# Kernel optimization log

Hardware: AMD Instinct MI355X
Metric: run time of the kernel (lower is better)

The kernel has to match this reference:

```python
import jax, jax.numpy as jnp
import numpy as np

EPS = 1e-6

def rmsnorm(x, w):
    # RMSNorm over last dim (head_dim), eps=1e-6, learned scale w
    return x * jax.lax.rsqrt(jnp.mean(x * x, axis=-1, keepdims=True) + EPS) * w

def setup_inputs() -> dict:
    key = jax.random.key(0)
    ks = jax.random.split(key, 8)
    B, L, D = 2, 256, 4096          # batch, new-chunk len, model dim
    H, Dh = 32, 128                  # heads, head_dim (H*Dh == D)
    SINK, LOCAL = 128, 4096          # attention-sink + sliding window
    S = SINK + LOCAL                 # fixed cache length
    s = 0.02
    return {
        "x": jax.random.normal(ks[0], (B, L, D), jnp.float32),
        "cache_k": jax.random.normal(ks[1], (B, S, H, Dh), jnp.float32),
        "cache_v": jax.random.normal(ks[2], (B, S, H, Dh), jnp.float32),
        "Wq": jax.random.normal(ks[3], (D, H * Dh), jnp.float32) * s,
        "Wk": jax.random.normal(ks[4], (D, H * Dh), jnp.float32) * s,
        "Wv": jax.random.normal(ks[5], (D, H * Dh), jnp.float32) * s,
        "Wo": jax.random.normal(ks[6], (H * Dh, D), jnp.float32) * s,
        "q_norm_w": jnp.ones((Dh,), jnp.float32),
        "k_norm_w": jnp.ones((Dh,), jnp.float32),
        "sink": 128,
    }

def reference(x, cache_k, cache_v, Wq, Wk, Wv, Wo, q_norm_w, k_norm_w, sink):
    B, L, D = x.shape
    S, H, Dh = cache_k.shape[1], cache_k.shape[2], cache_k.shape[3]
    # QKV projections (bias=False) + per-head RMSNorm on q and k
    q = rmsnorm((x @ Wq).reshape(B, L, H, Dh), q_norm_w)
    k = rmsnorm((x @ Wk).reshape(B, L, H, Dh), k_norm_w)
    v = (x @ Wv).reshape(B, L, H, Dh)
    # steady-state cache: keep sink tokens, roll local window left by L, write new chunk at tail
    new_k = jnp.concatenate([cache_k[:, :sink], cache_k[:, sink + L:], k], axis=1)  # [B,S,H,Dh]
    new_v = jnp.concatenate([cache_v[:, :sink], cache_v[:, sink + L:], v], axis=1)
    scale = 1.0 / jnp.sqrt(jnp.asarray(Dh, x.dtype))
    logits = jnp.einsum('blhd,bshd->bhls', q, new_k) * scale  # [B,H,L,S]
    # causal within the new chunk: query i sees cache positions j <= (S-L)+i
    i = jnp.arange(L)[:, None]
    j = jnp.arange(S)[None, :]
    mask = j <= (S - L) + i
    logits = jnp.where(mask[None, None], logits, jnp.finfo(logits.dtype).min)
    attn = jax.nn.softmax(logits, axis=-1)
    out = jnp.einsum('bhls,bshd->blhd', attn, new_v).reshape(B, L, H * Dh)
    return out @ Wo
```

## Files before the change

### kernel.cpp

```cpp
#include <hip/hip_runtime.h>
#include <stdint.h>
#include <stddef.h>

typedef unsigned short u16;
typedef __bf16 bf16x8 __attribute__((ext_vector_type(8)));
typedef float f32x4 __attribute__((ext_vector_type(4)));
typedef u16 u16x8 __attribute__((ext_vector_type(8)));

#define B_    2
#define L_    256
#define D_    4096
#define H_    32
#define DH_   128
#define SINK_ 128
#define S_    4224
#define WINS_ 3968
#define M_    512
#define SPLIT_ 4

__device__ __forceinline__ float bf2f(u16 u){
  union { float f; uint32_t i; } v; v.i = ((uint32_t)u) << 16; return v.f;
}
__device__ __forceinline__ u16 f2bf(float f){
  union { float f; uint32_t i; } v; v.f = f;
  return (u16)((v.i + 0x7fffu + ((v.i >> 16) & 1u)) >> 16);
}
__device__ __forceinline__ bf16x8 ld8(const u16* p){
  return __builtin_bit_cast(bf16x8, *(const u16x8*)p);
}
__device__ __forceinline__ bf16x8 ld8f(const float* p){
  f32x4 a = *(const f32x4*)p;
  f32x4 b = *(const f32x4*)(p + 4);
  u16x8 r;
  r[0] = f2bf(a[0]); r[1] = f2bf(a[1]); r[2] = f2bf(a[2]); r[3] = f2bf(a[3]);
  r[4] = f2bf(b[0]); r[5] = f2bf(b[1]); r[6] = f2bf(b[2]); r[7] = f2bf(b[3]);
  return __builtin_bit_cast(bf16x8, r);
}

__global__ void detect_k(const u16* __restrict__ x, uint32_t* __restrict__ flag){
  const int lane = threadIdx.x & 63;
  int bad = 0;
  for (int i = lane; i < 1024; i += 64){
    float v = bf2f(x[2 * i]);
    if (!(v * 0.0f == 0.0f) || fabsf(v) > 1e6f) bad = 1;
  }
#pragma unroll
  for (int m = 1; m < 64; m <<= 1) bad |= __shfl_xor(bad, m, 64);
  if (threadIdx.x == 0) *flag = (uint32_t)(bad ? 1 : 0);
}

__global__ __launch_bounds__(256) void transpose_k(const void* __restrict__ W,
                                                   u16* __restrict__ WT,
                                                   const uint32_t* __restrict__ flag){
  const int mode = (int)*flag;
  __shared__ u16 Ts[64 * 68];
  const int t  = threadIdx.x;
  const int k0 = blockIdx.x * 64;
  const int n0 = blockIdx.y * 64;
  const int r  = t >> 2;
  const int c  = (t & 3) * 8;
  const size_t rowoff = (size_t)(k0 + r) * 4096;
#pragma unroll
  for (int p = 0; p < 2; p++){
    const int cc = c + p * 32;
    u16x8 v;
    if (mode){
      const float* pf = (const float*)W + rowoff + n0 + cc;
      f32x4 a = *(const f32x4*)pf;
      f32x4 b = *(const f32x4*)(pf + 4);
      v[0] = f2bf(a[0]); v[1] = f2bf(a[1]); v[2] = f2bf(a[2]); v[3] = f2bf(a[3]);
      v[4] = f2bf(b[0]); v[5] = f2bf(b[1]); v[6] = f2bf(b[2]); v[7] = f2bf(b[3]);
    } else {
      v = *(const u16x8*)((const u16*)W + rowoff + n0 + cc);
    }
#pragma unroll
    for (int j = 0; j < 8; j++) Ts[r * 68 + cc + j] = v[j];
  }
  __syncthreads();
#pragma unroll
  for (int p = 0; p < 2; p++){
    const int kc = c + p * 32;
    u16x8 v;
#pragma unroll
    for (int j = 0; j < 8; j++) v[j] = Ts[(kc + j) * 68 + r];
    *(u16x8*)(WT + (size_t)(n0 + r) * 4096 + k0 + kc) = v;
  }
}

__global__ __launch_bounds__(256) void gemm_bt(const void* __restrict__ Ain,
                                               const u16* __restrict__ BT,
                                               void* __restrict__ Cout,
                                               const uint32_t* __restrict__ flag,
                                               int a_ext, int c_ext){
  const int mode = (int)*flag;
  const int a_f32 = a_ext & mode;
  const int c_f32 = c_ext & mode;

  const int n0 = blockIdx.x * 128;
  const int m0 = blockIdx.y * 64;

  __shared__ u16 As[64 * 32];
  __shared__ u16 Bs[128 * 32];

  const int t    = threadIdx.x;
  const int w    = t >> 6;
  const int lane = t & 63;
  const int wm   = w >> 1;
  const int wn   = w & 1;
  const int mq   = lane & 15;
  const int qd   = lane >> 4;

  f32x4 acc[2][4] = {};

  const size_t ga  = (size_t)(m0 + (t >> 2)) * 4096 + (t & 3) * 8;
  const size_t gb0 = (size_t)(n0 + (t >> 2)) * 4096 + (t & 3) * 8;
  const size_t gb1 = (size_t)(n0 + 64 + (t >> 2)) * 4096 + (t & 3) * 8;

  for (int kt = 0; kt < 128; kt++){
    const int k0 = kt * 32;
    u16x8 av;
    if (a_f32){
      const float* pa = (const float*)Ain + ga + k0;
      f32x4 a = *(const f32x4*)pa;
      f32x4 b = *(const f32x4*)(pa + 4);
      av[0] = f2bf(a[0]); av[1] = f2bf(a[1]); av[2] = f2bf(a[2]); av[3] = f2bf(a[3]);
      av[4] = f2bf(b[0]); av[5] = f2bf(b[1]); av[6] = f2bf(b[2]); av[7] = f2bf(b[3]);
    } else {
      av = *(const u16x8*)((const u16*)Ain + ga + k0);
    }
    u16x8 bv0 = *(const u16x8*)(BT + gb0 + k0);
    u16x8 bv1 = *(const u16x8*)(BT + gb1 + k0);
    __syncthreads();
    *(u16x8*)&As[t * 8]         = av;
    *(u16x8*)&Bs[t * 8]         = bv0;
    *(u16x8*)&Bs[(256 + t) * 8] = bv1;
    __syncthreads();

    bf16x8 af[2], bfr[4];
#pragma unroll
    for (int i = 0; i < 2; i++)
      af[i] = ld8(&As[(wm * 32 + i * 16 + mq) * 32 + qd * 8]);
#pragma unroll
    for (int j = 0; j < 4; j++)
      bfr[j] = ld8(&Bs[(wn * 64 + j * 16 + mq) * 32 + qd * 8]);
#pragma unroll
    for (int i = 0; i < 2; i++)
#pragma unroll
      for (int j = 0; j < 4; j++)
        acc[i][j] = __builtin_amdgcn_mfma_f32_16x16x32_bf16(af[i], bfr[j], acc[i][j], 0, 0, 0);
  }

#pragma unroll
  for (int i = 0; i < 2; i++)
#pragma unroll
    for (int j = 0; j < 4; j++)
#pragma unroll
      for (int r = 0; r < 4; r++){
        const int row = m0 + wm * 32 + i * 16 + qd * 4 + r;
        const int col = n0 + wn * 64 + j * 16 + mq;
        if (c_f32) ((float*)Cout)[(size_t)row * 4096 + col] = acc[i][j][r];
        else       ((u16*)Cout)[(size_t)row * 4096 + col]   = f2bf(acc[i][j][r]);
      }
}

__global__ __launch_bounds__(256) void rmsnorm_k(const u16* __restrict__ src,
                                                 u16* __restrict__ dst,
                                                 const void* __restrict__ wq,
                                                 const void* __restrict__ wk,
                                                 const uint32_t* __restrict__ flag){
  const int mode = (int)*flag;
  const int t = threadIdx.x, w = t >> 6, lane = t & 63;
  const size_t base = (size_t)blockIdx.y * (size_t)M_ * 4096;
  const int rid = blockIdx.x * 4 + w;
  const u16* s = src + base + (size_t)rid * 128 + lane * 2;
  u16*       d = dst + base + (size_t)rid * 128 + lane * 2;
  const void* wp = blockIdx.y ? wk : wq;
  float w0, w1;
  if (mode){ w0 = ((const float*)wp)[lane * 2]; w1 = ((const float*)wp)[lane * 2 + 1]; }
  else     { w0 = bf2f(((const u16*)wp)[lane * 2]); w1 = bf2f(((const u16*)wp)[lane * 2 + 1]); }
  const float f0 = bf2f(s[0]), f1 = bf2f(s[1]);
  float ss = f0 * f0 + f1 * f1;
#pragma unroll
  for (int m = 1; m < 64; m <<= 1) ss += __shfl_xor(ss, m, 64);
  const float rinv = rsqrtf(ss * (1.0f / 128.0f) + 1e-6f);
  d[0] = f2bf(f0 * rinv * w0);
  d[1] = f2bf(f1 * rinv * w1);
}

__global__ __launch_bounds__(1024) void attn_k(const u16* __restrict__ qn,
                                               const u16* __restrict__ kn,
                                               const u16* __restrict__ vnew,
                                               const void* __restrict__ ck,
                                               const void* __restrict__ cv,
                                               u16* __restrict__ ao,
                                               const uint32_t* __restrict__ flag){
  const int mode = (int)*flag;
  __shared__ __align__(16) unsigned char LDSB[61440];
  u16*   VTall = (u16*)LDSB;
  u16*   PBall = (u16*)LDSB + 4 * 5120;
  float* OB    = (float*)LDSB;
  float* ML    = (float*)(LDSB + 32768);

  const int t  = threadIdx.x;
  const int W  = t >> 6;
  const int sp = W >> 2;
  const int w  = W & 3;
  const int lane = t & 63;
  const int lt = t & 255;
  const int blk = blockIdx.x;
  const int b  = blk >> 7;
  const int h  = (blk >> 2) & 31;
  const int qt = blk & 3;
  const int q0 = qt * 64 + w * 16;
  const int mq = lane & 15;
  const int qd = lane >> 4;

  u16* VT = VTall + sp * (128 * 40);
  u16* pb = PBall + W * 640;

  bf16x8 aq[4];
  {
    const u16* qp = qn + ((size_t)(b * L_ + q0 + mq)) * 4096 + h * 128 + qd * 8;
#pragma unroll
    for (int kc = 0; kc < 4; kc++) aq[kc] = ld8(qp + kc * 32);
  }

  f32x4 oacc[8] = {};
  float mi[4], li[4];
#pragma unroll
  for (int r = 0; r < 4; r++){ mi[r] = -1e30f; li[r] = 0.f; }

  const int nchunks = (WINS_ + qt * 64 + 63) / 32 + 1;
  const int cpb = (nchunks + SPLIT_ - 1) / SPLIT_;
  const int sc_beg = sp * cpb;
  const int sc_end = (sc_beg + cpb < nchunks) ? (sc_beg + cpb) : nchunks;
  const float scale = 0.08838834764831845f;
  const float L2E = 1.4426950408889634f;

  const int dd = lt & 127, sg = lt >> 7;

  for (int scr = 0; scr < cpb; scr++){
    const int sc = sc_beg + scr;
    const int act = (sc < sc_end);
    const int s0 = sc * 32;

    u16 vv[16];
    if (act){
#pragma unroll
      for (int j = 0; j < 16; j++){
        const int s = s0 + sg * 16 + j;
        if (s >= WINS_){
          vv[j] = vnew[((size_t)(b * L_ + (s - WINS_)) << 12) + h * 128 + dd];
        } else {
          const int scc = (s < SINK_) ? s : (s + L_);
          const size_t off = ((((size_t)b * S_ + scc) * H_ + h) << 7) + dd;
          vv[j] = mode ? f2bf(((const float*)cv)[off]) : ((const u16*)cv)[off];
        }
      }
    }
    __syncthreads();
    if (act){
#pragma unroll
      for (int hv = 0; hv < 2; hv++){
        u16x8 pk;
#pragma unroll
        for (int j = 0; j < 8; j++) pk[j] = vv[hv * 8 + j];
        *(u16x8*)&VT[dd * 40 + sg * 16 + hv * 8] = pk;
      }
    }
    __syncthreads();

    if (act){
      float lg[2][4];
#pragma unroll
      for (int st = 0; st < 2; st++){
        const int s = s0 + st * 16 + mq;
        f32x4 a = {};
        if (s0 + st * 16 >= WINS_){
          const u16* kp = kn + ((size_t)(b * L_ + (s - WINS_)) << 12) + h * 128;
#pragma unroll
          for (int kc = 0; kc < 4; kc++)
            a = __builtin_amdgcn_mfma_f32_16x16x32_bf16(aq[kc], ld8(kp + kc * 32 + qd * 8), a, 0, 0, 0);
        } else if (mode){
          const int scc = (s < SINK_) ? s : (s + L_);
          const float* kp = (const float*)ck + ((((size_t)b * S_ + scc) * H_ + h) << 7);
#pragma unroll
          for (int kc = 0; kc < 4; kc++)
            a = __builtin_amdgcn_mfma_f32_16x16x32_bf16(aq[kc], ld8f(kp + kc * 32 + qd * 8), a, 0, 0, 0);
        } else {
          const int scc = (s < SINK_) ? s : (s + L_);
          const u16* kp = (const u16*)ck + ((((size_t)b * S_ + scc) * H_ + h) << 7);
#pragma unroll
          for (int kc = 0; kc < 4; kc++)
            a = __builtin_amdgcn_mfma_f32_16x16x32_bf16(aq[kc], ld8(kp + kc * 32 + qd * 8), a, 0, 0, 0);
        }
#pragma unroll
        for (int r = 0; r < 4; r++) lg[st][r] = a[r] * scale;
      }
      if (s0 + 31 > WINS_ + q0){
#pragma unroll
        for (int st = 0; st < 2; st++){
          const int s = s0 + st * 16 + mq;
#pragma unroll
          for (int r = 0; r < 4; r++)
            if (s > WINS_ + (q0 + qd * 4 + r)) lg[st][r] = -1e30f;
        }
      }
      float p[2][4];
#pragma unroll
      for (int r = 0; r < 4; r++){
        float mx = fmaxf(lg[0][r], lg[1][r]);
#pragma unroll
        for (int m = 1; m < 16; m <<= 1) mx = fmaxf(mx, __shfl_xor(mx, m, 64));
        const float mnew = fmaxf(mi[r], mx);
        const float alpha = exp2f((mi[r] - mnew) * L2E);
        mi[r] = mnew;
        float s_ = 0.f;
#pragma unroll
        for (int st = 0; st < 2; st++){
          p[st][r] = exp2f((lg[st][r] - mnew) * L2E);
          s_ += p[st][r];
        }
#pragma unroll
        for (int m = 1; m < 16; m <<= 1) s_ += __shfl_xor(s_, m, 64);
        li[r] = li[r] * alpha + s_;
#pragma unroll
        for (int nt = 0; nt < 8; nt++) oacc[nt][r] *= alpha;
      }
#pragma unroll
      for (int st = 0; st < 2; st++)
#pragma unroll
        for (int r = 0; r < 4; r++)
          pb[(qd * 4 + r) * 40 + st * 16 + mq] = f2bf(p[st][r]);
      asm volatile("" ::: "memory");
      u16x8 pr;
#pragma unroll
      for (int j = 0; j < 8; j++) pr[j] = pb[mq * 40 + qd * 8 + j];
      bf16x8 ap = __builtin_bit_cast(bf16x8, pr);
#pragma unroll
      for (int nt = 0; nt < 8; nt++){
        bf16x8 bv = ld8(&VT[(nt * 16 + mq) * 40 + qd * 8]);
        oacc[nt] = __builtin_amdgcn_mfma_f32_16x16x32_bf16(ap, bv, oacc[nt], 0, 0, 0);
      }
    }
  }

  __syncthreads();
  if (mq == 0){
#pragma unroll
    for (int r = 0; r < 4; r++){
      const int lr = w * 16 + qd * 4 + r;
      ML[(sp * 64 + lr) * 2 + 0] = mi[r];
      ML[(sp * 64 + lr) * 2 + 1] = li[r];
    }
  }
  __syncthreads();

  float gm[4], gl[4], wgt[4];
#pragma unroll
  for (int r = 0; r < 4; r++){
    const int lr = w * 16 + qd * 4 + r;
    float m_ = -1e30f;
#pragma unroll
    for (int p = 0; p < SPLIT_; p++) m_ = fmaxf(m_, ML[(p * 64 + lr) * 2 + 0]);
    gm[r] = m_;
    float l_ = 0.f;
#pragma unroll
    for (int p = 0; p < SPLIT_; p++)
      l_ += exp2f((ML[(p * 64 + lr) * 2 + 0] - m_) * L2E) * ML[(p * 64 + lr) * 2 + 1];
    gl[r] = l_;
    wgt[r] = exp2f((mi[r] - m_) * L2E);
  }

#pragma unroll
  for (int p = 0; p < SPLIT_; p++){
    if (sp == p){
#pragma unroll
      for (int nt = 0; nt < 8; nt++)
#pragma unroll
        for (int r = 0; r < 4; r++){
          const int off = (w * 16 + qd * 4 + r) * 128 + nt * 16 + mq;
          const float v = wgt[r] * oacc[nt][r];
          if (p == 0) OB[off] = v;
          else        OB[off] += v;
        }
    }
    __syncthreads();
  }

  if (sp == 0){
#pragma unroll
    for (int nt = 0; nt < 8; nt++)
#pragma unroll
      for (int r = 0; r < 4; r++){
        const int lr = w * 16 + qd * 4 + r;
        const int qrow = qt * 64 + lr;
        const float v = OB[lr * 128 + nt * 16 + mq] / gl[r];
        ao[((size_t)(b * L_ + qrow) << 12) + h * 128 + nt * 16 + mq] = f2bf(v);
      }
  }
}

extern "C" void kernel_launch(void* const* d_in, const int* in_sizes, int n_in,
                              void* d_out, int out_size, void* d_ws, size_t ws_size,
                              hipStream_t stream){
  (void)in_sizes; (void)n_in; (void)out_size; (void)ws_size;
  const void* x  = d_in[0];
  const void* ck = d_in[1];
  const void* cv = d_in[2];
  const void* Wq = d_in[3];
  const void* Wk = d_in[4];
  const void* Wv = d_in[5];
  const void* Wo = d_in[6];
  const void* qw = d_in[7];
  const void* kw = d_in[8];

  const size_t WT_E = 4096ull * 4096;
  const size_t BUF  = (size_t)M_ * 4096;

  uint32_t* flag = (uint32_t*)d_ws;
  u16* ws0 = (u16*)d_ws + 64;
  u16* WT  = ws0;
  u16* qkv = WT + WT_E;
  u16* qn  = qkv + 3 * BUF;
  u16* ao  = qn + 2 * BUF;

  detect_k<<<1, 64, 0, stream>>>((const u16*)x, flag);

  transpose_k<<<dim3(64, 64), 256, 0, stream>>>(Wq, WT, flag);
  gemm_bt<<<dim3(32, 8), 256, 0, stream>>>(x, WT, qkv, flag, 1, 0);
  transpose_k<<<dim3(64, 64), 256, 0, stream>>>(Wk, WT, flag);
  gemm_bt<<<dim3(32, 8), 256, 0, stream>>>(x, WT, qkv + BUF, flag, 1, 0);
  transpose_k<<<dim3(64, 64), 256, 0, stream>>>(Wv, WT, flag);
  gemm_bt<<<dim3(32, 8), 256, 0, stream>>>(x, WT, qkv + 2 * BUF, flag, 1, 0);

  rmsnorm_k<<<dim3(4096, 2), 256, 0, stream>>>(qkv, qn, qw, kw, flag);

  attn_k<<<dim3(256), 1024, 0, stream>>>(qn, qn + BUF, qkv + 2 * BUF,
                                         ck, cv, ao, flag);

  transpose_k<<<dim3(64, 64), 256, 0, stream>>>(Wo, WT, flag);
  gemm_bt<<<dim3(32, 8), 256, 0, stream>>>(ao, WT, d_out, flag, 0, 1);
}
```

Measured before the change: 1.389 ms.

## Batch QKV GEMMs into one launch, shrink GEMM tiles, retile attention with V prefetch

The three Q/K/V weight transposes are staged into separate workspace slices, and a single GEMM launch covers all three projections, falling back to sequential launches when the workspace is too small. The GEMM tile shrinks from 64x128 to 64x64, which quadruples the grid and fills more CUs. The attention kernel moves from 1024-thread blocks with 64 queries to 512-thread blocks with 32 queries and 512 blocks, and prefetches the next V chunk into registers during compute. The goal is better occupancy and latency hiding, at the cost of less operand reuse per tile and more workspace.

Result: no change. 1.409 ms (+1.4%).

```diff
diff --git a/kernel.cpp b/kernel.cpp
--- a/kernel.cpp
+++ b/kernel.cpp
@@ -87,20 +87,23 @@
   }
 }
 
-__global__ __launch_bounds__(256) void gemm_bt(const void* __restrict__ Ain,
-                                               const u16* __restrict__ BT,
-                                               void* __restrict__ Cout,
-                                               const uint32_t* __restrict__ flag,
-                                               int a_ext, int c_ext){
+__global__ __launch_bounds__(256) void gemm64_k(const void* __restrict__ Ain,
+                                                const u16* __restrict__ BT3,
+                                                void* __restrict__ Cout,
+                                                const uint32_t* __restrict__ flag,
+                                                int a_ext, int c_ext){
   const int mode = (int)*flag;
   const int a_f32 = a_ext & mode;
   const int c_f32 = c_ext & mode;
 
-  const int n0 = blockIdx.x * 128;
+  const int bx = blockIdx.x;
+  const int wi = bx >> 6;
+  const int n0 = (bx & 63) * 64;
   const int m0 = blockIdx.y * 64;
+  const u16* BT = BT3 + (size_t)wi * (4096ull * 4096);
 
   __shared__ u16 As[64 * 32];
-  __shared__ u16 Bs[128 * 32];
+  __shared__ u16 Bs[64 * 32];
 
   const int t    = threadIdx.x;
   const int w    = t >> 6;
@@ -110,11 +113,10 @@
   const int mq   = lane & 15;
   const int qd   = lane >> 4;
 
-  f32x4 acc[2][4] = {};
-
-  const size_t ga  = (size_t)(m0 + (t >> 2)) * 4096 + (t & 3) * 8;
-  const size_t gb0 = (size_t)(n0 + (t >> 2)) * 4096 + (t & 3) * 8;
-  const size_t gb1 = (size_t)(n0 + 64 + (t >> 2)) * 4096 + (t & 3) * 8;
+  f32x4 acc[2][2] = {};
+
+  const size_t ga = (size_t)(m0 + (t >> 2)) * 4096 + (t & 3) * 8;
+  const size_t gb = (size_t)(n0 + (t >> 2)) * 4096 + (t & 3) * 8;
 
   for (int kt = 0; kt < 128; kt++){
     const int k0 = kt * 32;
@@ -128,38 +130,37 @@
     } else {
       av = *(const u16x8*)((const u16*)Ain + ga + k0);
     }
-    u16x8 bv0 = *(const u16x8*)(BT + gb0 + k0);
-    u16x8 bv1 = *(const u16x8*)(BT + gb1 + k0);
+    u16x8 bv = *(const u16x8*)(BT + gb + k0);
     __syncthreads();
-    *(u16x8*)&As[t * 8]         = av;
-    *(u16x8*)&Bs[t * 8]         = bv0;
-    *(u16x8*)&Bs[(256 + t) * 8] = bv1;
+    *(u16x8*)&As[t * 8] = av;
+    *(u16x8*)&Bs[t * 8] = bv;
     __syncthreads();
 
-    bf16x8 af[2], bfr[4];
+    bf16x8 af[2], bfr[2];
 #pragma unroll
     for (int i = 0; i < 2; i++)
       af[i] = ld8(&As[(wm * 32 + i * 16 + mq) * 32 + qd * 8]);
 #pragma unroll
-    for (int j = 0; j < 4; j++)
-      bfr[j] = ld8(&Bs[(wn * 64 + j * 16 + mq) * 32 + qd * 8]);
+    for (int j = 0; j < 2; j++)
+      bfr[j] = ld8(&Bs[(wn * 32 + j * 16 + mq) * 32 + qd * 8]);
 #pragma unroll
     for (int i = 0; i < 2; i++)
 #pragma unroll
-      for (int j = 0; j < 4; j++)
+      for (int j = 0; j < 2; j++)
         acc[i][j] = __builtin_amdgcn_mfma_f32_16x16x32_bf16(af[i], bfr[j], acc[i][j], 0, 0, 0);
   }
 
+  u16* cu = (u16*)Cout + (size_t)wi * ((size_t)M_ * 4096);
 #pragma unroll
   for (int i = 0; i < 2; i++)
 #pragma unroll
-    for (int j = 0; j < 4; j++)
+    for (int j = 0; j < 2; j++)
 #pragma unroll
       for (int r = 0; r < 4; r++){
         const int row = m0 + wm * 32 + i * 16 + qd * 4 + r;
-        const int col = n0 + wn * 64 + j * 16 + mq;
+        const int col = n0 + wn * 32 + j * 16 + mq;
         if (c_f32) ((float*)Cout)[(size_t)row * 4096 + col] = acc[i][j][r];
-        else       ((u16*)Cout)[(size_t)row * 4096 + col]   = f2bf(acc[i][j][r]);
+        else       cu[(size_t)row * 4096 + col]             = f2bf(acc[i][j][r]);
       }
 }
 
@@ -187,31 +188,31 @@
   d[1] = f2bf(f1 * rinv * w1);
 }
 
-__global__ __launch_bounds__(1024) void attn_k(const u16* __restrict__ qn,
-                                               const u16* __restrict__ kn,
-                                               const u16* __restrict__ vnew,
-                                               const void* __restrict__ ck,
-                                               const void* __restrict__ cv,
-                                               u16* __restrict__ ao,
-                                               const uint32_t* __restrict__ flag){
+__global__ __launch_bounds__(512, 4) void attn_k(const u16* __restrict__ qn,
+                                                 const u16* __restrict__ kn,
+                                                 const u16* __restrict__ vnew,
+                                                 const void* __restrict__ ck,
+                                                 const void* __restrict__ cv,
+                                                 u16* __restrict__ ao,
+                                                 const uint32_t* __restrict__ flag){
   const int mode = (int)*flag;
-  __shared__ __align__(16) unsigned char LDSB[61440];
+  __shared__ __align__(16) unsigned char LDSB[51200];
   u16*   VTall = (u16*)LDSB;
-  u16*   PBall = (u16*)LDSB + 4 * 5120;
+  u16*   PBall = (u16*)(LDSB + 40960);
   float* OB    = (float*)LDSB;
-  float* ML    = (float*)(LDSB + 32768);
+  float* ML    = (float*)(LDSB + 16384);
 
   const int t  = threadIdx.x;
   const int W  = t >> 6;
-  const int sp = W >> 2;
-  const int w  = W & 3;
+  const int sp = W >> 1;
+  const int w  = W & 1;
   const int lane = t & 63;
-  const int lt = t & 255;
+  const int lt = t & 127;
   const int blk = blockIdx.x;
-  const int b  = blk >> 7;
-  const int h  = (blk >> 2) & 31;
-  const int qt = blk & 3;
-  const int q0 = qt * 64 + w * 16;
+  const int b  = blk >> 8;
+  const int h  = (blk >> 3) & 31;
+  const int qt = blk & 7;
+  const int q0 = qt * 32 + w * 16;
   const int mq = lane & 15;
   const int qd = lane >> 4;
 
@@ -230,45 +231,51 @@
 #pragma unroll
   for (int r = 0; r < 4; r++){ mi[r] = -1e30f; li[r] = 0.f; }
 
-  const int nchunks = (WINS_ + qt * 64 + 63) / 32 + 1;
+  const int nchunks = (WINS_ + qt * 32 + 63) / 32;
   const int cpb = (nchunks + SPLIT_ - 1) / SPLIT_;
   const int sc_beg = sp * cpb;
   const int sc_end = (sc_beg + cpb < nchunks) ? (sc_beg + cpb) : nchunks;
   const float scale = 0.08838834764831845f;
   const float L2E = 1.4426950408889634f;
 
-  const int dd = lt & 127, sg = lt >> 7;
+  const int dd = lt;
+  u16x8 vv[4];
+
+  auto loadV = [&](int sc){
+    const int s0c = sc * 32;
+#pragma unroll
+    for (int c = 0; c < 4; c++){
+#pragma unroll
+      for (int j = 0; j < 8; j++){
+        const int s = s0c + c * 8 + j;
+        u16 val;
+        if (s >= WINS_){
+          val = vnew[((size_t)(b * L_ + (s - WINS_)) << 12) + h * 128 + dd];
+        } else {
+          const int scc = (s < SINK_) ? s : (s + L_);
+          const size_t off = ((((size_t)b * S_ + scc) * H_ + h) << 7) + dd;
+          val = mode ? f2bf(((const float*)cv)[off]) : ((const u16*)cv)[off];
+        }
+        vv[c][j] = val;
+      }
+    }
+  };
+
+  if (sc_beg < sc_end) loadV(sc_beg);
 
   for (int scr = 0; scr < cpb; scr++){
     const int sc = sc_beg + scr;
     const int act = (sc < sc_end);
     const int s0 = sc * 32;
 
-    u16 vv[16];
-    if (act){
-#pragma unroll
-      for (int j = 0; j < 16; j++){
-        const int s = s0 + sg * 16 + j;
-        if (s >= WINS_){
-          vv[j] = vnew[((size_t)(b * L_ + (s - WINS_)) << 12) + h * 128 + dd];
-        } else {
-          const int scc = (s < SINK_) ? s : (s + L_);
-          const size_t off = ((((size_t)b * S_ + scc) * H_ + h) << 7) + dd;
-          vv[j] = mode ? f2bf(((const float*)cv)[off]) : ((const u16*)cv)[off];
-        }
-      }
-    }
     __syncthreads();
     if (act){
 #pragma unroll
-      for (int hv = 0; hv < 2; hv++){
-        u16x8 pk;
-#pragma unroll
-        for (int j = 0; j < 8; j++) pk[j] = vv[hv * 8 + j];
-        *(u16x8*)&VT[dd * 40 + sg * 16 + hv * 8] = pk;
-      }
+      for (int c = 0; c < 4; c++)
+        *(u16x8*)&VT[dd * 40 + c * 8] = vv[c];
     }
     __syncthreads();
+    if (sc + 1 < sc_end) loadV(sc + 1);
 
     if (act){
       float lg[2][4];
@@ -350,24 +357,23 @@
 #pragma unroll
     for (int r = 0; r < 4; r++){
       const int lr = w * 16 + qd * 4 + r;
-      ML[(sp * 64 + lr) * 2 + 0] = mi[r];
-      ML[(sp * 64 + lr) * 2 + 1] = li[r];
+      ML[(sp * 32 + lr) * 2 + 0] = mi[r];
+      ML[(sp * 32 + lr) * 2 + 1] = li[r];
     }
   }
   __syncthreads();
 
-  float gm[4], gl[4], wgt[4];
+  float gl[4], wgt[4];
 #pragma unroll
   for (int r = 0; r < 4; r++){
     const int lr = w * 16 + qd * 4 + r;
     float m_ = -1e30f;
 #pragma unroll
-    for (int p = 0; p < SPLIT_; p++) m_ = fmaxf(m_, ML[(p * 64 + lr) * 2 + 0]);
-    gm[r] = m_;
+    for (int p = 0; p < SPLIT_; p++) m_ = fmaxf(m_, ML[(p * 32 + lr) * 2 + 0]);
     float l_ = 0.f;
 #pragma unroll
     for (int p = 0; p < SPLIT_; p++)
-      l_ += exp2f((ML[(p * 64 + lr) * 2 + 0] - m_) * L2E) * ML[(p * 64 + lr) * 2 + 1];
+      l_ += exp2f((ML[(p * 32 + lr) * 2 + 0] - m_) * L2E) * ML[(p * 32 + lr) * 2 + 1];
     gl[r] = l_;
     wgt[r] = exp2f((mi[r] - m_) * L2E);
   }
@@ -394,7 +400,7 @@
 #pragma unroll
       for (int r = 0; r < 4; r++){
         const int lr = w * 16 + qd * 4 + r;
-        const int qrow = qt * 64 + lr;
+        const int qrow = qt * 32 + lr;
         const float v = OB[lr * 128 + nt * 16 + mq] / gl[r];
         ao[((size_t)(b * L_ + qrow) << 12) + h * 128 + nt * 16 + mq] = f2bf(v);
       }
@@ -404,7 +410,7 @@
 extern "C" void kernel_launch(void* const* d_in, const int* in_sizes, int n_in,
                               void* d_out, int out_size, void* d_ws, size_t ws_size,
                               hipStream_t stream){
-  (void)in_sizes; (void)n_in; (void)out_size; (void)ws_size;
+  (void)in_sizes; (void)n_in; (void)out_size;
   const void* x  = d_in[0];
   const void* ck = d_in[1];
   const void* cv = d_in[2];
@@ -420,25 +426,47 @@
 
   uint32_t* flag = (uint32_t*)d_ws;
   u16* ws0 = (u16*)d_ws + 64;
-  u16* WT  = ws0;
-  u16* qkv = WT + WT_E;
-  u16* qn  = qkv + 3 * BUF;
-  u16* ao  = qn + 2 * BUF;
 
   detect_k<<<1, 64, 0, stream>>>((const u16*)x, flag);
 
-  transpose_k<<<dim3(64, 64), 256, 0, stream>>>(Wq, WT, flag);
-  gemm_bt<<<dim3(32, 8), 256, 0, stream>>>(x, WT, qkv, flag, 1, 0);
-  transpose_k<<<dim3(64, 64), 256, 0, stream>>>(Wk, WT, flag);
-  gemm_bt<<<dim3(32, 8), 256, 0, stream>>>(x, WT, qkv + BUF, flag, 1, 0);
-  transpose_k<<<dim3(64, 64), 256, 0, stream>>>(Wv, WT, flag);
-  gemm_bt<<<dim3(32, 8), 256, 0, stream>>>(x, WT, qkv + 2 * BUF, flag, 1, 0);
-
-  rmsnorm_k<<<dim3(4096, 2), 256, 0, stream>>>(qkv, qn, qw, kw, flag);
-
-  attn_k<<<dim3(256), 1024, 0, stream>>>(qn, qn + BUF, qkv + 2 * BUF,
-                                         ck, cv, ao, flag);
-
-  transpose_k<<<dim3(64, 64), 256, 0, stream>>>(Wo, WT, flag);
-  gemm_bt<<<dim3(32, 8), 256, 0, stream>>>(ao, WT, d_out, flag, 0, 1);
-}
+  const size_t need_fused = 128 + (3 * WT_E + 6 * BUF) * 2;
+  if (ws_size >= need_fused){
+    u16* WT3 = ws0;
+    u16* qkv = WT3 + 3 * WT_E;
+    u16* qn  = qkv + 3 * BUF;
+    u16* ao  = qn + 2 * BUF;
+
+    transpose_k<<<dim3(64, 64), 256, 0, stream>>>(Wq, WT3, flag);
+    transpose_k<<<dim3(64, 64), 256, 0, stream>>>(Wk, WT3 + WT_E, flag);
+    transpose_k<<<dim3(64, 64), 256, 0, stream>>>(Wv, WT3 + 2 * WT_E, flag);
+    gemm64_k<<<dim3(192, 8), 256, 0, stream>>>(x, WT3, qkv, flag, 1, 0);
+
+    rmsnorm_k<<<dim3(4096, 2), 256, 0, stream>>>(qkv, qn, qw, kw, flag);
+
+    attn_k<<<dim3(512), 512, 0, stream>>>(qn, qn + BUF, qkv + 2 * BUF,
+                                          ck, cv, ao, flag);
+
+    transpose_k<<<dim3(64, 64), 256, 0, stream>>>(Wo, WT3, flag);
+    gemm64_k<<<dim3(64, 8), 256, 0, stream>>>(ao, WT3, d_out, flag, 0, 1);
+  } else {
+    u16* WT  = ws0;
+    u16* qkv = WT + WT_E;
+    u16* qn  = qkv + 3 * BUF;
+    u16* ao  = qn + 2 * BUF;
+
+    transpose_k<<<dim3(64, 64), 256, 0, stream>>>(Wq, WT, flag);
+    gemm64_k<<<dim3(64, 8), 256, 0, stream>>>(x, WT, qkv, flag, 1, 0);
+    transpose_k<<<dim3(64, 64), 256, 0, stream>>>(Wk, WT, flag);
+    gemm64_k<<<dim3(64, 8), 256, 0, stream>>>(x, WT, qkv + BUF, flag, 1, 0);
+    transpose_k<<<dim3(64, 64), 256, 0, stream>>>(Wv, WT, flag);
+    gemm64_k<<<dim3(64, 8), 256, 0, stream>>>(x, WT, qkv + 2 * BUF, flag, 1, 0);
+
+    rmsnorm_k<<<dim3(4096, 2), 256, 0, stream>>>(qkv, qn, qw, kw, flag);
+
+    attn_k<<<dim3(512), 512, 0, stream>>>(qn, qn + BUF, qkv + 2 * BUF,
+                                          ck, cv, ao, flag);
+
+    transpose_k<<<dim3(64, 64), 256, 0, stream>>>(Wo, WT, flag);
+    gemm64_k<<<dim3(64, 8), 256, 0, stream>>>(ao, WT, d_out, flag, 0, 1);
+  }
+}
```
